# Kernel optimization log

Measured on AMD Instinct MI355X. Metric: run time of the kernel, lower is better.

Reference implementation:

```python
import jax, jax.numpy as jnp
import numpy as np
from jax import lax

# 8 neighbor offsets of the Moore neighborhood (matches neighbors_roll_axes)
OFFS = [(i, j) for i in range(-1, 2) for j in range(-1, 2) if not (i == 0 and j == 0)]


def _neighbors(g):
    # g: [B,1,H,W]; toroidal shifts
    return [jnp.roll(g, (i, j), axis=(2, 3)) for i, j in OFFS]


def _binary_step(gb):
    # Conway rule on boolean grid: alive if sum==3 or (alive and sum==2)
    s = sum(n.astype(jnp.int32) for n in _neighbors(gb))
    return (s == 3) | (gb & (s == 2))


def _prob_step(p):
    # P(next alive) = P(exactly 3 of 8 neighbors alive) + P(exactly 2 alive) * p
    # Computed via a count-distribution DP over the 8 independent Bernoulli
    # neighbors -- mathematically identical to the C(8,2)+C(8,3)=84 enumerated
    # products in the torch code, but O(8) fused elementwise passes.
    z = jnp.zeros_like(p)
    c0, c1, c2, c3 = jnp.ones_like(p), z, z, z  # P(count==k); >=4 absorbed
    for q in _neighbors(p):
        c3 = c3 * (1 - q) + c2 * q
        c2 = c2 * (1 - q) + c1 * q
        c1 = c1 * (1 - q) + c0 * q
        c0 = c0 * (1 - q)
    return c3 + c2 * p


def _cconv(x, w, b, pad):
    # circular ('wrap') padding conv, NCHW/OIHW
    if pad:
        x = jnp.pad(x, ((0, 0), (0, 0), (pad, pad), (pad, pad)), mode='wrap')
    y = lax.conv_general_dilated(x, w, (1, 1), 'VALID',
                                 dimension_numbers=('NCHW', 'OIHW', 'NCHW'))
    return y + b[None, :, None, None]


def _block(x, xp, params):
    w1, b1, w2, b2, w3, b3, w4, b4 = params
    # stencil features computed under no_grad in the original
    xp_bin = lax.stop_gradient(xp > 0.5)
    x_pred_bin = _binary_step(xp_bin)
    x_pred = lax.stop_gradient(_prob_step(lax.stop_gradient(xp)))
    h = jnp.concatenate([x, xp, xp_bin.astype(x.dtype), x_pred,
                         x_pred_bin.astype(x.dtype)], axis=1)  # [B,5,H,W]
    h = jax.nn.relu(_cconv(h, w1, b1, 2))
    h = jax.nn.relu(_cconv(h, w2, b2, 1))
    h = jax.nn.relu(_cconv(h, w3, b3, 0))
    return jax.nn.sigmoid(_cconv(h, w4, b4, 1))


def setup_inputs() -> dict:
    key = jax.random.key(0)
    ks = jax.random.split(key, 6)
    B, H, W = 4, 256, 256
    x = jax.random.uniform(ks[0], (B, 1, H, W), jnp.float32)

    def wi(k, shape):
        fan_in = shape[1] * shape[2] * shape[3]
        return (jax.random.normal(k, shape, jnp.float32) / np.sqrt(fan_in)).astype(jnp.float32)

    w1 = wi(ks[1], (256, 5, 5, 5));   b1 = jnp.zeros((256,), jnp.float32)
    w2 = wi(ks[2], (256, 256, 3, 3)); b2 = jnp.zeros((256,), jnp.float32)
    w3 = wi(ks[3], (256, 256, 1, 1)); b3 = jnp.zeros((256,), jnp.float32)
    w4 = wi(ks[4], (1, 256, 3, 3));   b4 = jnp.zeros((1,), jnp.float32)
    return {"x": x, "w1": w1, "b1": b1, "w2": w2, "b2": b2,
            "w3": w3, "b3": b3, "w4": w4, "b4": b4, "n_it": 5}


def reference(x, w1, b1, w2, b2, w3, b3, w4, b4, n_it):
    params = (w1, b1, w2, b2, w3, b3, w4, b4)
    xp = x
    for _ in range(n_it):
        xp = _block(x, xp, params)
    return xp
```

## Files before the change

### kernel.cpp

```cpp
#include <hip/hip_runtime.h>
#include <hip/hip_bf16.h>


#define NPIX (4 * 256 * 256)

typedef double v4d __attribute__((ext_vector_type(4)));

__global__ __launch_bounds__(64) void probe_mode(int* __restrict__ modep)
{
    int lr = threadIdx.x & 15;
    v4d p1 = {}, p2 = {};
    p1 = __builtin_amdgcn_mfma_f64_16x16x4f64((double)lr, 1.0, p1, 0, 0, 0);
    p2 = __builtin_amdgcn_mfma_f64_16x16x4f64(1.0, (double)lr, p2, 0, 0, 0);
    double v1 = __shfl(p1[0], 16);
    double v2 = __shfl(p2[0], 16);
    if (threadIdx.x == 0)
        *modep = (v1 == 16.0) ? 0 : (v1 == 4.0) ? 1 : (v2 == 16.0) ? 2 : 3;
}

__global__ __launch_bounds__(256) void xinit_kernel(
    const float* __restrict__ x, double* __restrict__ xp64)
{
    int p = blockIdx.x * 256 + threadIdx.x;
    xp64[p] = (double)x[p];
}

__global__ __launch_bounds__(256) void stencil_strip(
    const float* __restrict__ x, const double* __restrict__ xp,
    double* __restrict__ h0, size_t h0_is,
    int job0, int ns_shift, int R)
{
    int slot = blockIdx.y;
    int j = job0 + slot;
    int img = j >> ns_shift;
    int r0 = (j & ((1 << ns_shift) - 1)) * R;
    int pbase = img << 16;
    int y = (r0 - 4 + blockIdx.x) & 255;
    int col = threadIdx.x;
    double q[8];
    int s = 0, idx = 0;
    #pragma unroll
    for (int i = -1; i <= 1; ++i)
        #pragma unroll
        for (int jj = -1; jj <= 1; ++jj) {
            if (i == 0 && jj == 0) continue;
            int ys = (y - i) & 255, xs = (col - jj) & 255;
            double v = xp[pbase + ((ys << 8) | xs)];
            q[idx++] = v;
            s += (v > 0.5) ? 1 : 0;
        }
    double c = xp[pbase + ((y << 8) | col)];
    bool alive = c > 0.5;
    bool binnext = (s == 3) || (alive && s == 2);
    double c0 = 1.0, c1 = 0.0, c2 = 0.0, c3 = 0.0;
    #pragma unroll
    for (int k = 0; k < 8; ++k) {
        double qq = q[k], r = 1.0 - qq;
        c3 = c3 * r + c2 * qq;
        c2 = c2 * r + c1 * qq;
        c1 = c1 * r + c0 * qq;
        c0 = c0 * r;
    }
    double xpred = c3 + c2 * c;
    double* o = h0 + slot * h0_is + ((size_t)blockIdx.x * 256 + col) * 8;
    o[0] = (double)x[pbase + ((y << 8) | col)];
    o[1] = c;
    o[2] = alive ? 1.0 : 0.0;
    o[3] = xpred;
    o[4] = binnext ? 1.0 : 0.0;
    o[5] = 0.0; o[6] = 0.0; o[7] = 0.0;
}

template<int CIN, int TK, int KH, int KW>
__global__ __launch_bounds__(512, 6) void conv_gemm(
    const double* __restrict__ A, size_t a_is,
    const double* __restrict__ Wp,
    const float* __restrict__ bias,
    double* __restrict__ O, size_t o_is,
    int delta, const int* __restrict__ modep)
{
    constexpr int PW = KW / 2, PH = KH / 2;
    constexpr int CHUNKS = CIN / TK;
    constexpr int NCH = KH * KW * CHUNKS;
    __shared__ double Asmem[2][TK][66];
    __shared__ double Wsmem[2][TK][66];

    const double* Ai = A + blockIdx.z * a_is;
    double* Oi = O + blockIdx.z * o_is;
    const int mode = *modep;

    const int tid = threadIdx.x;
    const int pm0 = blockIdx.x * 64;
    const int on0 = blockIdx.y * 64;
    const int wave = tid >> 6, lane = tid & 63;
    const bool prod = wave >= 4;
    if (!prod) asm volatile("s_setprio 1");

    const int ptid = tid & 255;
    constexpr int LPP = TK / 2;
    constexpr int PPR = 256 / LPP;
    constexpr int ROUNDS = 64 / PPR;
    const int part = ptid % LPP;
    const int pixA = ptid / LPP;
    const int wrow = ptid >> 5;
    const int wcol = (ptid & 31) << 1;

    const int lq = lane >> 4, lr = lane & 15;
    const int wr = ((wave >> 1) & 1) * 32;
    const int wc = (wave & 1) * 32;

    v4d acc[2][2] = {};

    auto stage = [&](int ch, int buf) {
        int tap = ch / CHUNKS, cc = ch % CHUNKS;
        int dy = tap / KW - PH, dx = tap % KW - PW;
        int c0 = cc * TK;
        int kglob = tap * CIN + c0;
        #pragma unroll
        for (int r = 0; r < TK / 8; ++r) {
            int row = r * 8 + wrow;
            *(double2*)&Wsmem[buf][row][wcol] =
                *(const double2*)&Wp[(size_t)(kglob + row) * 256 + on0 + wcol];
        }
        #pragma unroll
        for (int r = 0; r < ROUNDS; ++r) {
            int pix = r * PPR + pixA;
            int pl = pm0 + pix;
            int yl = pl >> 8, col = pl & 255;
            int xs = (col + dx) & 255;
            int srcpx = ((yl + dy + delta) << 8) | xs;
            double2 v = *(const double2*)(Ai + (size_t)srcpx * CIN + c0 + part * 2);
            Asmem[buf][part * 2 + 0][pix] = v.x;
            Asmem[buf][part * 2 + 1][pix] = v.y;
        }
    };

    if (prod) stage(0, 0);
    __syncthreads();
    for (int ch = 0; ch < NCH; ++ch) {
        const int cur = ch & 1;
        if (prod) {
            if (ch + 1 < NCH) stage(ch + 1, cur ^ 1);
        } else {
            #pragma unroll
            for (int k0 = 0; k0 < TK / 4; ++k0) {
                const int kk = k0 * 4 + lq;
                double a[2], b[2];
                a[0] = Asmem[cur][kk][wr + lr];
                a[1] = Asmem[cur][kk][wr + 16 + lr];
                b[0] = Wsmem[cur][kk][wc + lr];
                b[1] = Wsmem[cur][kk][wc + 16 + lr];
                #pragma unroll
                for (int rt = 0; rt < 2; ++rt)
                    #pragma unroll
                    for (int ct = 0; ct < 2; ++ct)
                        acc[rt][ct] = __builtin_amdgcn_mfma_f64_16x16x4f64(
                            a[rt], b[ct], acc[rt][ct], 0, 0, 0);
            }
        }
        __syncthreads();
    }

    if (!prod) {
        #pragma unroll
        for (int rt = 0; rt < 2; ++rt)
            #pragma unroll
            for (int ct = 0; ct < 2; ++ct)
                #pragma unroll
                for (int i = 0; i < 4; ++i) {
                    int hq = lq * 4 + i, hi = i * 4 + lq;
                    int rl = (mode == 0) ? hq : (mode == 1) ? hi : lr;
                    int cl = (mode <= 1) ? lr : (mode == 2) ? hq : hi;
                    int px = pm0 + wr + rt * 16 + rl;
                    int oc = on0 + wc + ct * 16 + cl;
                    Oi[(size_t)px * 256 + oc] =
                        fmax(acc[rt][ct][i] + (double)bias[oc], 0.0);
                }
    }
}

__global__ __launch_bounds__(512, 6) void conv2_gemm(
    const double* __restrict__ A, size_t a_is,
    const double* __restrict__ Wp,
    const float* __restrict__ bias,
    double* __restrict__ O, size_t o_is,
    const int* __restrict__ modep)
{
    __shared__ double Asmem[2][8][66];
    __shared__ double Wsmem[2][24][66];

    const double* Ai = A + blockIdx.z * a_is;
    double* Oi = O + blockIdx.z * o_is;
    const int mode = *modep;

    const int tid = threadIdx.x;
    const int pm0 = blockIdx.x * 64;
    const int on0 = blockIdx.y * 64;
    const int yrow = pm0 >> 8;
    const int col0 = pm0 & 255;
    const int wave = tid >> 6, lane = tid & 63;
    const bool prod = wave >= 4;
    if (!prod) asm volatile("s_setprio 1");

    const int ptid = tid & 255;
    const int lq = lane >> 4, lr = lane & 15;
    const int wr = ((wave >> 1) & 1) * 32;
    const int wc = (wave & 1) * 32;

    v4d acc[2][2] = {};

    auto stage = [&](int ch, int buf) {
        int dy = ch >> 5;
        int cc = ch & 31;
        int c0 = cc * 8;
        int srow = yrow + dy;
        {
            int px = ptid >> 2, pp = ptid & 3;
            int xs = (col0 - 1 + px) & 255;
            double2 v = *(const double2*)(
                Ai + (size_t)((srow << 8) | xs) * 256 + c0 + pp * 2);
            Asmem[buf][pp * 2 + 0][px] = v.x;
            Asmem[buf][pp * 2 + 1][px] = v.y;
            if (ptid < 8) {
                int t2 = 256 + ptid;
                int px2 = t2 >> 2, pp2 = t2 & 3;
                int xs2 = (col0 - 1 + px2) & 255;
                double2 v2 = *(const double2*)(
                    Ai + (size_t)((srow << 8) | xs2) * 256 + c0 + pp2 * 2);
                Asmem[buf][pp2 * 2 + 0][px2] = v2.x;
                Asmem[buf][pp2 * 2 + 1][px2] = v2.y;
            }
        }
        #pragma unroll
        for (int i = 0; i < 3; ++i) {
            int row = i * 8 + (ptid >> 5);
            int cp = (ptid & 31) << 1;
            int tap = dy * 3 + (row >> 3);
            int k = tap * 256 + c0 + (row & 7);
            *(double2*)&Wsmem[buf][row][cp] =
                *(const double2*)&Wp[(size_t)k * 256 + on0 + cp];
        }
    };

    if (prod) stage(0, 0);
    __syncthreads();
    for (int ch = 0; ch < 96; ++ch) {
        const int cur = ch & 1;
        if (prod) {
            if (ch + 1 < 96) stage(ch + 1, cur ^ 1);
        } else {
            #pragma unroll
            for (int dx = 0; dx < 3; ++dx)
                #pragma unroll
                for (int k0 = 0; k0 < 2; ++k0) {
                    const int kA = k0 * 4 + lq;
                    const int kW = dx * 8 + k0 * 4 + lq;
                    double a[2], b[2];
                    a[0] = Asmem[cur][kA][dx + wr + lr];
                    a[1] = Asmem[cur][kA][dx + wr + 16 + lr];
                    b[0] = Wsmem[cur][kW][wc + lr];
                    b[1] = Wsmem[cur][kW][wc + 16 + lr];
                    #pragma unroll
                    for (int rt = 0; rt < 2; ++rt)
                        #pragma unroll
                        for (int ct = 0; ct < 2; ++ct)
                            acc[rt][ct] = __builtin_amdgcn_mfma_f64_16x16x4f64(
                                a[rt], b[ct], acc[rt][ct], 0, 0, 0);
                }
        }
        __syncthreads();
    }

    if (!prod) {
        #pragma unroll
        for (int rt = 0; rt < 2; ++rt)
            #pragma unroll
            for (int ct = 0; ct < 2; ++ct)
                #pragma unroll
                for (int i = 0; i < 4; ++i) {
                    int hq = lq * 4 + i, hi = i * 4 + lq;
                    int rl = (mode == 0) ? hq : (mode == 1) ? hi : lr;
                    int cl = (mode <= 1) ? lr : (mode == 2) ? hq : hi;
                    int px = pm0 + wr + rt * 16 + rl;
                    int oc = on0 + wc + ct * 16 + cl;
                    Oi[(size_t)px * 256 + oc] =
                        fmax(acc[rt][ct][i] + (double)bias[oc], 0.0);
                }
    }
}

__global__ __launch_bounds__(256) void conv4_sig(
    const double* __restrict__ H3, size_t h3_is,
    const float* __restrict__ w4, const float* __restrict__ b4,
    float* __restrict__ out, double* __restrict__ xp_new,
    int job0, int ns_shift, int R)
{
    __shared__ double w4s[2304];
    int tid = threadIdx.x;
    for (int i = tid; i < 2304; i += 256) w4s[i] = (double)w4[i];
    __syncthreads();
    int slot = blockIdx.y;
    int j = job0 + slot;
    int img = j >> ns_shift;
    int r0 = (j & ((1 << ns_shift) - 1)) * R;
    const double* H3i = H3 + slot * h3_is;
    int pbase = img << 16;
    int lane = tid & 63, wv = tid >> 6;
    int p0 = blockIdx.x * 64 + wv * 16;
    for (int pi = 0; pi < 16; ++pi) {
        int pl = p0 + pi;
        int yl = pl >> 8, col = pl & 255;
        double acc = 0.0;
        #pragma unroll
        for (int tap = 0; tap < 9; ++tap) {
            int row = yl + tap / 3 - 1 + 1;
            int xs = (col + tap % 3 - 1) & 255;
            const double* src = H3i + (size_t)((row << 8) | xs) * 256;
            #pragma unroll
            for (int jj = 0; jj < 4; ++jj) {
                int c = lane + 64 * jj;
                acc = fma(src[c], w4s[c * 9 + tap], acc);
            }
        }
        #pragma unroll
        for (int off = 32; off; off >>= 1) acc += __shfl_xor(acc, off, 64);
        if (lane == 0) {
            double v = acc + (double)b4[0];
            double s = 1.0 / (1.0 + exp(-v));
            int p = pbase + (((r0 + yl) << 8) | col);
            out[p] = (float)s;
            xp_new[p] = s;
        }
    }
}

__global__ void repack_w1(const float* __restrict__ w1, double* __restrict__ W1p) {
    int t = blockIdx.x * 256 + threadIdx.x;
    if (t >= 25 * 8 * 256) return;
    int oc = t & 255, cin = (t >> 8) & 7, tap = t >> 11;
    W1p[t] = (cin < 5) ? (double)w1[oc * 125 + cin * 25 + tap] : 0.0;
}
__global__ void repack_w2(const float* __restrict__ w2, double* __restrict__ W2p) {
    int t = blockIdx.x * 256 + threadIdx.x;
    if (t >= 9 * 256 * 256) return;
    int oc = t & 255, cin = (t >> 8) & 255, tap = t >> 16;
    W2p[t] = (double)w2[((oc << 8) | cin) * 9 + tap];
}
__global__ void repack_w3(const float* __restrict__ w3, double* __restrict__ W3p) {
    int t = blockIdx.x * 256 + threadIdx.x;
    if (t >= 256 * 256) return;
    int oc = t & 255, cin = t >> 8;
    W3p[t] = (double)w3[oc * 256 + cin];
}

extern "C" void kernel_launch(void* const* d_in, const int* in_sizes, int n_in,
                              void* d_out, int out_size, void* d_ws, size_t ws_size,
                              hipStream_t stream)
{
    const float* x  = (const float*)d_in[0];
    const float* w1 = (const float*)d_in[1];
    const float* b1 = (const float*)d_in[2];
    const float* w2 = (const float*)d_in[3];
    const float* b2 = (const float*)d_in[4];
    const float* w3 = (const float*)d_in[5];
    const float* b3 = (const float*)d_in[6];
    const float* w4 = (const float*)d_in[7];
    const float* b4 = (const float*)d_in[8];
    float* out = (float*)d_out;

    char* ws = (char*)d_ws;
    double* W1p = (double*)(ws);
    double* W2p = (double*)(ws + 409600ull);
    double* W3p = (double*)(ws + 5128192ull);
    double* xpA = (double*)(ws + 5652480ull);
    double* xpB = (double*)(ws + 7749632ull);
    int*   modep = (int*)(ws + 9846784ull);
    char*  bufs = ws + 9847040ull;
    const size_t base_need = 9847040ull;
    const size_t ROWD  = 524288ull;
    const size_t ROWH0 = 16384ull;

    const int cand_r[14] = {64, 128, 256, 64, 32, 64, 16, 32, 16, 8, 8, 4, 4, 2};
    const int cand_g[14] = { 4,   2,   1,  3,  4,  2,  4,  2,  2, 4, 2, 2, 1, 1};
    int R = 2, G = 1;
    for (int ci = 0; ci < 14; ++ci) {
        int r = cand_r[ci], g = cand_g[ci];
        size_t need = base_need + (size_t)g *
            ((size_t)(r + 8) * ROWH0 + (size_t)(2 * r + 6) * ROWD);
        if (ws_size >= need) { R = r; G = g; break; }
    }
    int ns_shift = 0;
    while ((256 >> ns_shift) != R) ++ns_shift;
    const int NSTRIP = 256 / R;
    const int jobs = 4 * NSTRIP;

    double* h0 = (double*)bufs;
    double* h1 = (double*)(bufs + (size_t)G * (R + 8) * ROWH0);
    double* h2 = (double*)((char*)h1 + (size_t)G * (R + 4) * ROWD);
    double* h3 = h1;
    const size_t h0_is = (size_t)(R + 8) * 256 * 8;
    const size_t h1_is = (size_t)(R + 4) * 256 * 256;
    const size_t h2_is = (size_t)(R + 2) * 256 * 256;

    probe_mode<<<1, 64, 0, stream>>>(modep);
    repack_w1<<<200, 256, 0, stream>>>(w1, W1p);
    repack_w2<<<2304, 256, 0, stream>>>(w2, W2p);
    repack_w3<<<256, 256, 0, stream>>>(w3, W3p);
    xinit_kernel<<<NPIX / 256, 256, 0, stream>>>(x, xpA);

    for (int it = 0; it < 5; ++it) {
        const double* xp_rd = (it & 1) ? xpB : xpA;
        double*       xp_wr = (it & 1) ? xpA : xpB;
        for (int j0 = 0; j0 < jobs; j0 += G) {
            int g = (jobs - j0 < G) ? (jobs - j0) : G;
            stencil_strip<<<dim3(R + 8, g), 256, 0, stream>>>(
                x, xp_rd, h0, h0_is, j0, ns_shift, R);
            conv_gemm<8, 8, 5, 5><<<dim3((R + 4) * 4, 4, g), 512, 0, stream>>>(
                h0, h0_is, W1p, b1, h1, h1_is, 2, modep);
            conv2_gemm<<<dim3((R + 2) * 4, 4, g), 512, 0, stream>>>(
                h1, h1_is, W2p, b2, h2, h2_is, modep);
            conv_gemm<256, 16, 1, 1><<<dim3((R + 2) * 4, 4, g), 512, 0, stream>>>(
                h2, h2_is, W3p, b3, h3, h1_is, 0, modep);
            conv4_sig<<<dim3(R * 4, g), 256, 0, stream>>>(
                h3, h1_is, w4, b4, out, xp_wr, j0, ns_shift, R);
        }
    }
}
```

Baseline: 42.49 ms.

## Drop producer/consumer wave split; all 8 waves compute 128-pixel tiles

The conv GEMM kernels previously split 512 threads into 4 producer waves that staged tiles and 4 consumer waves that ran FP64 MFMAs. Now all 8 waves compute on a 128x64 output tile. Each wave loads the next chunk into registers, runs MFMAs on the current shared buffer at raised priority, then writes the staged registers to shared memory. This doubles MFMA-active waves and halves the grid along pixels, improving weight reuse per block, at the cost of more registers per thread and one barrier per chunk without dedicated loader waves.

```diff
diff --git a/kernel.cpp b/kernel.cpp
--- a/kernel.cpp
+++ b/kernel.cpp
@@ -82,7 +82,13 @@
     constexpr int PW = KW / 2, PH = KH / 2;
     constexpr int CHUNKS = CIN / TK;
     constexpr int NCH = KH * KW * CHUNKS;
-    __shared__ double Asmem[2][TK][66];
+    constexpr int LPP = TK / 2;
+    constexpr int NA = 128 * LPP;
+    constexpr int NW = TK * 32;
+    constexpr int NT = NA + NW;
+    constexpr int TPT = (NT + 511) / 512;
+
+    __shared__ double Asmem[2][TK][130];
     __shared__ double Wsmem[2][TK][66];
 
     const double* Ai = A + blockIdx.z * a_is;
@@ -90,66 +96,192 @@
     const int mode = *modep;
 
     const int tid = threadIdx.x;
-    const int pm0 = blockIdx.x * 64;
+    const int pm0 = blockIdx.x * 128;
     const int on0 = blockIdx.y * 64;
+    const int yl0 = pm0 >> 8;
+    const int c0l = pm0 & 255;
     const int wave = tid >> 6, lane = tid & 63;
-    const bool prod = wave >= 4;
-    if (!prod) asm volatile("s_setprio 1");
-
-    const int ptid = tid & 255;
-    constexpr int LPP = TK / 2;
-    constexpr int PPR = 256 / LPP;
-    constexpr int ROUNDS = 64 / PPR;
-    const int part = ptid % LPP;
-    const int pixA = ptid / LPP;
-    const int wrow = ptid >> 5;
-    const int wcol = (ptid & 31) << 1;
-
     const int lq = lane >> 4, lr = lane & 15;
-    const int wr = ((wave >> 1) & 1) * 32;
+    const int wr = (wave >> 1) * 32;
     const int wc = (wave & 1) * 32;
 
     v4d acc[2][2] = {};
-
-    auto stage = [&](int ch, int buf) {
-        int tap = ch / CHUNKS, cc = ch % CHUNKS;
+    double2 st[TPT];
+
+    auto load_tasks = [&](int ch) {
+        int tap = ch / CHUNKS, cc = ch - tap * CHUNKS;
         int dy = tap / KW - PH, dx = tap % KW - PW;
         int c0 = cc * TK;
         int kglob = tap * CIN + c0;
-        #pragma unroll
-        for (int r = 0; r < TK / 8; ++r) {
-            int row = r * 8 + wrow;
-            *(double2*)&Wsmem[buf][row][wcol] =
-                *(const double2*)&Wp[(size_t)(kglob + row) * 256 + on0 + wcol];
-        }
-        #pragma unroll
-        for (int r = 0; r < ROUNDS; ++r) {
-            int pix = r * PPR + pixA;
-            int pl = pm0 + pix;
-            int yl = pl >> 8, col = pl & 255;
-            int xs = (col + dx) & 255;
-            int srcpx = ((yl + dy + delta) << 8) | xs;
-            double2 v = *(const double2*)(Ai + (size_t)srcpx * CIN + c0 + part * 2);
-            Asmem[buf][part * 2 + 0][pix] = v.x;
-            Asmem[buf][part * 2 + 1][pix] = v.y;
+        int srow = yl0 + dy + delta;
+        #pragma unroll
+        for (int i = 0; i < TPT; ++i) {
+            int u = tid + i * 512;
+            if (NT % 512 == 0 || u < NT) {
+                if (u < NA) {
+                    int px = u / LPP, pp = u % LPP;
+                    int xs = (c0l + px + dx) & 255;
+                    st[i] = *(const double2*)(
+                        Ai + (size_t)((srow << 8) | xs) * CIN + c0 + pp * 2);
+                } else {
+                    int u2 = u - NA;
+                    int row = u2 >> 5, cp = (u2 & 31) << 1;
+                    st[i] = *(const double2*)&Wp[
+                        (size_t)(kglob + row) * 256 + on0 + cp];
+                }
+            }
         }
     };
-
-    if (prod) stage(0, 0);
+    auto write_tasks = [&](int buf) {
+        #pragma unroll
+        for (int i = 0; i < TPT; ++i) {
+            int u = tid + i * 512;
+            if (NT % 512 == 0 || u < NT) {
+                if (u < NA) {
+                    int px = u / LPP, pp = u % LPP;
+                    Asmem[buf][pp * 2 + 0][px] = st[i].x;
+                    Asmem[buf][pp * 2 + 1][px] = st[i].y;
+                } else {
+                    int u2 = u - NA;
+                    int row = u2 >> 5, cp = (u2 & 31) << 1;
+                    *(double2*)&Wsmem[buf][row][cp] = st[i];
+                }
+            }
+        }
+    };
+
+    load_tasks(0);
+    write_tasks(0);
     __syncthreads();
     for (int ch = 0; ch < NCH; ++ch) {
         const int cur = ch & 1;
-        if (prod) {
-            if (ch + 1 < NCH) stage(ch + 1, cur ^ 1);
-        } else {
+        if (ch + 1 < NCH) load_tasks(ch + 1);
+        __builtin_amdgcn_s_setprio(1);
+        #pragma unroll
+        for (int k0 = 0; k0 < TK / 4; ++k0) {
+            const int kk = k0 * 4 + lq;
+            double a[2], b[2];
+            a[0] = Asmem[cur][kk][wr + lr];
+            a[1] = Asmem[cur][kk][wr + 16 + lr];
+            b[0] = Wsmem[cur][kk][wc + lr];
+            b[1] = Wsmem[cur][kk][wc + 16 + lr];
             #pragma unroll
-            for (int k0 = 0; k0 < TK / 4; ++k0) {
-                const int kk = k0 * 4 + lq;
+            for (int rt = 0; rt < 2; ++rt)
+                #pragma unroll
+                for (int ct = 0; ct < 2; ++ct)
+                    acc[rt][ct] = __builtin_amdgcn_mfma_f64_16x16x4f64(
+                        a[rt], b[ct], acc[rt][ct], 0, 0, 0);
+        }
+        __builtin_amdgcn_s_setprio(0);
+        if (ch + 1 < NCH) write_tasks(cur ^ 1);
+        __syncthreads();
+    }
+
+    #pragma unroll
+    for (int rt = 0; rt < 2; ++rt)
+        #pragma unroll
+        for (int ct = 0; ct < 2; ++ct)
+            #pragma unroll
+            for (int i = 0; i < 4; ++i) {
+                int hq = lq * 4 + i, hi = i * 4 + lq;
+                int rl = (mode == 0) ? hq : (mode == 1) ? hi : lr;
+                int cl = (mode <= 1) ? lr : (mode == 2) ? hq : hi;
+                int px = pm0 + wr + rt * 16 + rl;
+                int oc = on0 + wc + ct * 16 + cl;
+                Oi[(size_t)px * 256 + oc] =
+                    fmax(acc[rt][ct][i] + (double)bias[oc], 0.0);
+            }
+}
+
+__global__ __launch_bounds__(512, 6) void conv2_gemm(
+    const double* __restrict__ A, size_t a_is,
+    const double* __restrict__ Wp,
+    const float* __restrict__ bias,
+    double* __restrict__ O, size_t o_is,
+    const int* __restrict__ modep)
+{
+    __shared__ double Asmem[2][8][130];
+    __shared__ double Wsmem[2][24][66];
+    constexpr int NA = 520;
+    constexpr int NT = 1288;
+
+    const double* Ai = A + blockIdx.z * a_is;
+    double* Oi = O + blockIdx.z * o_is;
+    const int mode = *modep;
+
+    const int tid = threadIdx.x;
+    const int pm0 = blockIdx.x * 128;
+    const int on0 = blockIdx.y * 64;
+    const int yrow = pm0 >> 8;
+    const int col0 = pm0 & 255;
+    const int wave = tid >> 6, lane = tid & 63;
+    const int lq = lane >> 4, lr = lane & 15;
+    const int wr = (wave >> 1) * 32;
+    const int wc = (wave & 1) * 32;
+
+    v4d acc[2][2] = {};
+    double2 st[3];
+
+    auto load_tasks = [&](int ch) {
+        int dy = ch >> 5;
+        int cc = ch & 31;
+        int c0 = cc * 8;
+        int srow = yrow + dy;
+        #pragma unroll
+        for (int i = 0; i < 3; ++i) {
+            int u = tid + i * 512;
+            if (u < NT) {
+                if (u < NA) {
+                    int px = u >> 2, pp = u & 3;
+                    int xs = (col0 - 1 + px) & 255;
+                    st[i] = *(const double2*)(
+                        Ai + (size_t)((srow << 8) | xs) * 256 + c0 + pp * 2);
+                } else {
+                    int u2 = u - NA;
+                    int row = u2 >> 5, cp = (u2 & 31) << 1;
+                    int tap = dy * 3 + (row >> 3);
+                    int k = tap * 256 + c0 + (row & 7);
+                    st[i] = *(const double2*)&Wp[(size_t)k * 256 + on0 + cp];
+                }
+            }
+        }
+    };
+    auto write_tasks = [&](int buf) {
+        #pragma unroll
+        for (int i = 0; i < 3; ++i) {
+            int u = tid + i * 512;
+            if (u < NT) {
+                if (u < NA) {
+                    int px = u >> 2, pp = u & 3;
+                    Asmem[buf][pp * 2 + 0][px] = st[i].x;
+                    Asmem[buf][pp * 2 + 1][px] = st[i].y;
+                } else {
+                    int u2 = u - NA;
+                    int row = u2 >> 5, cp = (u2 & 31) << 1;
+                    *(double2*)&Wsmem[buf][row][cp] = st[i];
+                }
+            }
+        }
+    };
+
+    load_tasks(0);
+    write_tasks(0);
+    __syncthreads();
+    for (int ch = 0; ch < 96; ++ch) {
+        const int cur = ch & 1;
+        if (ch + 1 < 96) load_tasks(ch + 1);
+        __builtin_amdgcn_s_setprio(1);
+        #pragma unroll
+        for (int dx = 0; dx < 3; ++dx)
+            #pragma unroll
+            for (int k0 = 0; k0 < 2; ++k0) {
+                const int kA = k0 * 4 + lq;
+                const int kW = dx * 8 + k0 * 4 + lq;
                 double a[2], b[2];
-                a[0] = Asmem[cur][kk][wr + lr];
-                a[1] = Asmem[cur][kk][wr + 16 + lr];
-                b[0] = Wsmem[cur][kk][wc + lr];
-                b[1] = Wsmem[cur][kk][wc + 16 + lr];
+                a[0] = Asmem[cur][kA][dx + wr + lr];
+                a[1] = Asmem[cur][kA][dx + wr + 16 + lr];
+                b[0] = Wsmem[cur][kW][wc + lr];
+                b[1] = Wsmem[cur][kW][wc + 16 + lr];
                 #pragma unroll
                 for (int rt = 0; rt < 2; ++rt)
                     #pragma unroll
@@ -157,136 +289,25 @@
                         acc[rt][ct] = __builtin_amdgcn_mfma_f64_16x16x4f64(
                             a[rt], b[ct], acc[rt][ct], 0, 0, 0);
             }
-        }
+        __builtin_amdgcn_s_setprio(0);
+        if (ch + 1 < 96) write_tasks(cur ^ 1);
         __syncthreads();
     }
 
-    if (!prod) {
-        #pragma unroll
-        for (int rt = 0; rt < 2; ++rt)
+    #pragma unroll
+    for (int rt = 0; rt < 2; ++rt)
+        #pragma unroll
+        for (int ct = 0; ct < 2; ++ct)
             #pragma unroll
-            for (int ct = 0; ct < 2; ++ct)
-                #pragma unroll
-                for (int i = 0; i < 4; ++i) {
-                    int hq = lq * 4 + i, hi = i * 4 + lq;
-                    int rl = (mode == 0) ? hq : (mode == 1) ? hi : lr;
-                    int cl = (mode <= 1) ? lr : (mode == 2) ? hq : hi;
-                    int px = pm0 + wr + rt * 16 + rl;
-                    int oc = on0 + wc + ct * 16 + cl;
-                    Oi[(size_t)px * 256 + oc] =
-                        fmax(acc[rt][ct][i] + (double)bias[oc], 0.0);
-                }
-    }
-}
-
-__global__ __launch_bounds__(512, 6) void conv2_gemm(
-    const double* __restrict__ A, size_t a_is,
-    const double* __restrict__ Wp,
-    const float* __restrict__ bias,
-    double* __restrict__ O, size_t o_is,
-    const int* __restrict__ modep)
-{
-    __shared__ double Asmem[2][8][66];
-    __shared__ double Wsmem[2][24][66];
-
-    const double* Ai = A + blockIdx.z * a_is;
-    double* Oi = O + blockIdx.z * o_is;
-    const int mode = *modep;
-
-    const int tid = threadIdx.x;
-    const int pm0 = blockIdx.x * 64;
-    const int on0 = blockIdx.y * 64;
-    const int yrow = pm0 >> 8;
-    const int col0 = pm0 & 255;
-    const int wave = tid >> 6, lane = tid & 63;
-    const bool prod = wave >= 4;
-    if (!prod) asm volatile("s_setprio 1");
-
-    const int ptid = tid & 255;
-    const int lq = lane >> 4, lr = lane & 15;
-    const int wr = ((wave >> 1) & 1) * 32;
-    const int wc = (wave & 1) * 32;
-
-    v4d acc[2][2] = {};
-
-    auto stage = [&](int ch, int buf) {
-        int dy = ch >> 5;
-        int cc = ch & 31;
-        int c0 = cc * 8;
-        int srow = yrow + dy;
-        {
-            int px = ptid >> 2, pp = ptid & 3;
-            int xs = (col0 - 1 + px) & 255;
-            double2 v = *(const double2*)(
-                Ai + (size_t)((srow << 8) | xs) * 256 + c0 + pp * 2);
-            Asmem[buf][pp * 2 + 0][px] = v.x;
-            Asmem[buf][pp * 2 + 1][px] = v.y;
-            if (ptid < 8) {
-                int t2 = 256 + ptid;
-                int px2 = t2 >> 2, pp2 = t2 & 3;
-                int xs2 = (col0 - 1 + px2) & 255;
-                double2 v2 = *(const double2*)(
-                    Ai + (size_t)((srow << 8) | xs2) * 256 + c0 + pp2 * 2);
-                Asmem[buf][pp2 * 2 + 0][px2] = v2.x;
-                Asmem[buf][pp2 * 2 + 1][px2] = v2.y;
-            }
-        }
-        #pragma unroll
-        for (int i = 0; i < 3; ++i) {
-            int row = i * 8 + (ptid >> 5);
-            int cp = (ptid & 31) << 1;
-            int tap = dy * 3 + (row >> 3);
-            int k = tap * 256 + c0 + (row & 7);
-            *(double2*)&Wsmem[buf][row][cp] =
-                *(const double2*)&Wp[(size_t)k * 256 + on0 + cp];
-        }
-    };
-
-    if (prod) stage(0, 0);
-    __syncthreads();
-    for (int ch = 0; ch < 96; ++ch) {
-        const int cur = ch & 1;
-        if (prod) {
-            if (ch + 1 < 96) stage(ch + 1, cur ^ 1);
-        } else {
-            #pragma unroll
-            for (int dx = 0; dx < 3; ++dx)
-                #pragma unroll
-                for (int k0 = 0; k0 < 2; ++k0) {
-                    const int kA = k0 * 4 + lq;
-                    const int kW = dx * 8 + k0 * 4 + lq;
-                    double a[2], b[2];
-                    a[0] = Asmem[cur][kA][dx + wr + lr];
-                    a[1] = Asmem[cur][kA][dx + wr + 16 + lr];
-                    b[0] = Wsmem[cur][kW][wc + lr];
-                    b[1] = Wsmem[cur][kW][wc + 16 + lr];
-                    #pragma unroll
-                    for (int rt = 0; rt < 2; ++rt)
-                        #pragma unroll
-                        for (int ct = 0; ct < 2; ++ct)
-                            acc[rt][ct] = __builtin_amdgcn_mfma_f64_16x16x4f64(
-                                a[rt], b[ct], acc[rt][ct], 0, 0, 0);
-                }
-        }
-        __syncthreads();
-    }
-
-    if (!prod) {
-        #pragma unroll
-        for (int rt = 0; rt < 2; ++rt)
-            #pragma unroll
-            for (int ct = 0; ct < 2; ++ct)
-                #pragma unroll
-                for (int i = 0; i < 4; ++i) {
-                    int hq = lq * 4 + i, hi = i * 4 + lq;
-                    int rl = (mode == 0) ? hq : (mode == 1) ? hi : lr;
-                    int cl = (mode <= 1) ? lr : (mode == 2) ? hq : hi;
-                    int px = pm0 + wr + rt * 16 + rl;
-                    int oc = on0 + wc + ct * 16 + cl;
-                    Oi[(size_t)px * 256 + oc] =
-                        fmax(acc[rt][ct][i] + (double)bias[oc], 0.0);
-                }
-    }
+            for (int i = 0; i < 4; ++i) {
+                int hq = lq * 4 + i, hi = i * 4 + lq;
+                int rl = (mode == 0) ? hq : (mode == 1) ? hi : lr;
+                int cl = (mode <= 1) ? lr : (mode == 2) ? hq : hi;
+                int px = pm0 + wr + rt * 16 + rl;
+                int oc = on0 + wc + ct * 16 + cl;
+                Oi[(size_t)px * 256 + oc] =
+                    fmax(acc[rt][ct][i] + (double)bias[oc], 0.0);
+            }
 }
 
 __global__ __launch_bounds__(256) void conv4_sig(
@@ -415,11 +436,11 @@
             int g = (jobs - j0 < G) ? (jobs - j0) : G;
             stencil_strip<<<dim3(R + 8, g), 256, 0, stream>>>(
                 x, xp_rd, h0, h0_is, j0, ns_shift, R);
-            conv_gemm<8, 8, 5, 5><<<dim3((R + 4) * 4, 4, g), 512, 0, stream>>>(
+            conv_gemm<8, 8, 5, 5><<<dim3((R + 4) * 2, 4, g), 512, 0, stream>>>(
                 h0, h0_is, W1p, b1, h1, h1_is, 2, modep);
-            conv2_gemm<<<dim3((R + 2) * 4, 4, g), 512, 0, stream>>>(
+            conv2_gemm<<<dim3((R + 2) * 2, 4, g), 512, 0, stream>>>(
                 h1, h1_is, W2p, b2, h2, h2_is, modep);
-            conv_gemm<256, 16, 1, 1><<<dim3((R + 2) * 4, 4, g), 512, 0, stream>>>(
+            conv_gemm<256, 16, 1, 1><<<dim3((R + 2) * 2, 4, g), 512, 0, stream>>>(
                 h2, h2_is, W3p, b3, h3, h1_is, 0, modep);
             conv4_sig<<<dim3(R * 4, g), 256, 0, stream>>>(
                 h3, h1_is, w4, b4, out, xp_wr, j0, ns_shift, R);
```

New measurement: 42.05 ms. No clear change (-1.0%).
